# Optimization experiments

Hardware: AMD Instinct MI355X
Metric: run time of the kernel (lower is better)

The kernel has to match this reference:

```python
import jax, jax.numpy as jnp
import numpy as np

N = 50000          # masked node count
E = 800000         # edges (avg degree 16)
IN_DIM, GCN_DIM, REL_DIM, TRAIN_DIM, OUT_DIM = 3, 128, 64, 128, 2
BATCHES = 1


def setup_inputs() -> dict:
    key = jax.random.key(0)
    ks = jax.random.split(key, 16)
    s = 0.05
    return {
        "features": jax.random.normal(ks[0], (N, IN_DIM), jnp.float32),
        "edge_index": jax.random.randint(ks[1], (2, E), 0, N, dtype=jnp.int32),
        "trainOT": jax.random.normal(ks[2], (TRAIN_DIM,), jnp.float32),
        "W1": jax.random.normal(ks[3], (IN_DIM, GCN_DIM), jnp.float32) * s,
        "b1": jnp.zeros((GCN_DIM,), jnp.float32),
        "W2": jax.random.normal(ks[4], (GCN_DIM, GCN_DIM), jnp.float32) * s,
        "b2": jnp.zeros((GCN_DIM,), jnp.float32),
        "Wq": jax.random.normal(ks[5], (GCN_DIM, REL_DIM), jnp.float32) * s,
        "bq": jnp.zeros((REL_DIM,), jnp.float32),
        "Wk": jax.random.normal(ks[6], (TRAIN_DIM, REL_DIM), jnp.float32) * s,
        "bk": jnp.zeros((REL_DIM,), jnp.float32),
        "Wv": jax.random.normal(ks[7], (GCN_DIM, TRAIN_DIM), jnp.float32) * s,
        "bv": jnp.zeros((TRAIN_DIM,), jnp.float32),
        "Ws": jax.random.normal(ks[8], (TRAIN_DIM, OUT_DIM * N), jnp.float32) * s,
        "bs": jnp.zeros((OUT_DIM * N,), jnp.float32),
    }


def _gcn_conv(x, W, b, src, dst, n):
    """PyG GCNConv: h = D^-1/2 (A+I) D^-1/2 (x W) + b (self-loops already in src/dst)."""
    h = x @ W                                                  # [n, d_out]
    ones = jnp.ones(src.shape[0], dtype=x.dtype)
    deg = jax.ops.segment_sum(ones, dst, num_segments=n)      # in-degree incl. self-loop
    dinv = jnp.where(deg > 0, jax.lax.rsqrt(deg), 0.0)
    norm = dinv[src] * dinv[dst]                               # [E+n]
    msg = h[src] * norm[:, None]                               # gather (dominant traffic)
    return jax.ops.segment_sum(msg, dst, num_segments=n) + b   # scatter-add


def reference(features, edge_index, trainOT, W1, b1, W2, b2, Wq, bq, Wk, bk, Wv, bv, Ws, bs):
    n = features.shape[0]
    loop = jnp.arange(n, dtype=edge_index.dtype)
    src = jnp.concatenate([edge_index[0], loop])
    dst = jnp.concatenate([edge_index[1], loop])

    h1 = jax.nn.relu(_gcn_conv(features, W1, b1, src, dst, n))   # gcn1 + relu
    h2 = _gcn_conv(h1, W2, b2, src, dst, n)                      # gcn2

    q = h2 @ Wq + bq                                             # [n, rel]
    v = h2 @ Wv + bv                                             # [n, train]
    k = trainOT @ Wk + bk                                        # [rel]
    scale = jnp.asarray(Wq.shape[1], q.dtype) ** 0.5
    rel = jax.nn.sigmoid((q @ k) / scale)                        # [n]
    summed_idea = (rel[:, None] * v).sum(axis=0)                 # [train]
    new_trainOT = trainOT + summed_idea
    speak = new_trainOT @ Ws + bs                                # [out_dim * num_nodes]
    out = speak.reshape(BATCHES, -1, OUT_DIM)
    return out, new_trainOT
```

## Files before the change

kernel.cpp:

```cpp
#include <hip/hip_runtime.h>
#include <math.h>

#define O_RPD    (0)
#define O_RPS    (256*1024)
#define O_DINV   (512*1024)
#define O_SMALL  (768*1024)
#define O_Y      (1024*1024)
#define O_RELW   (1280*1024)
#define O_REL    (1536*1024)
#define O_GHD    (1792*1024)
#define O_GHS    (2048*1024)
#define O_GOD    (2304*1024)
#define O_GOS    (2560*1024)
#define O_BSD    (2816*1024)
#define O_BSS    (2944*1024)
#define O_PART   (3072*1024)
#define O_XS     (3712*1024)
#define O_G1     (4608*1024)
#define O_SRTD   (5632*1024)
#define O_SRTS   (9216*1024)
#define O_COLD   (12544*1024)
#define O_COLS   (16128*1024)

#define NCHUNK 256
#define ZBLOCKS 1024

static __device__ __forceinline__ int blockExclScan256(int v, volatile int* lds, int t) {
    int lane = t & 63, wid = t >> 6;
    int incl = v;
#pragma unroll
    for (int off = 1; off < 64; off <<= 1) {
        int n = __shfl_up(incl, off);
        if (lane >= off) incl += n;
    }
    if (lane == 63) lds[wid] = incl;
    __syncthreads();
    if (t == 0) {
        int s = 0;
#pragma unroll
        for (int i = 0; i < 4; ++i) { int x = lds[i]; lds[i] = s; s += x; }
    }
    __syncthreads();
    return lds[wid] + incl - v;
}

__global__ void k_hist(const int* __restrict__ eidx, int* __restrict__ ghD,
                       int* __restrict__ ghS,
                       const float* __restrict__ trainOT, const float* __restrict__ Wq,
                       const float* __restrict__ bq, const float* __restrict__ Wk,
                       const float* __restrict__ bk, const float* __restrict__ W2,
                       const float* __restrict__ b2, float* __restrict__ small,
                       int E, int CS, int NB) {
    int b = blockIdx.x, t = threadIdx.x;
    if (b == NCHUNK) {
        if (blockIdx.y) return;
        __shared__ float kv[64];
        __shared__ float wqk[128];
        __shared__ float fred[256];
        if (t < 64) {
            float acc = bk[t];
            for (int j = 0; j < 128; ++j) acc += trainOT[j] * Wk[j * 64 + t];
            kv[t] = acc;
        }
        __syncthreads();
        if (t < 128) {
            float aq = 0.f;
            for (int c2 = 0; c2 < 64; ++c2) aq += Wq[t * 64 + c2] * kv[c2];
            wqk[t] = aq;
        }
        fred[t] = (t < 64) ? bq[t] * kv[t] : 0.f;
        __syncthreads();
        for (int off = 128; off >= 1; off >>= 1) { if (t < off) fred[t] += fred[t + off]; __syncthreads(); }
        float bqs = fred[0];
        __syncthreads();
        if (t < 128) {
            float a2 = 0.f;
            for (int j = 0; j < 128; ++j) a2 += W2[t * 128 + j] * wqk[j];
            small[t] = a2;
        }
        fred[t] = (t < 128) ? b2[t] * wqk[t] : 0.f;
        __syncthreads();
        for (int off = 128; off >= 1; off >>= 1) { if (t < off) fred[t] += fred[t + off]; __syncthreads(); }
        if (t == 0) small[128] = bqs + fred[0];
        return;
    }
    __shared__ int lh[256];
    const int* arr = blockIdx.y ? eidx : (eidx + E);
    int* gh = blockIdx.y ? ghS : ghD;
    lh[t] = 0; __syncthreads();
    int s = b * CS, e = min(E, s + CS);
    for (int i = s + t; i < e; i += 256) atomicAdd(&lh[arr[i] >> 8], 1);
    __syncthreads();
    if (t < NB) gh[t * NCHUNK + b] = lh[t];
}

__global__ void k_bstart(const int* __restrict__ ghD, const int* __restrict__ ghS,
                         int* __restrict__ bsD, int* __restrict__ bsS, int NB) {
    __shared__ int lds1[4];
    __shared__ int lds2[4];
    int t = threadIdx.x;
    int vD = 0, vS = 0;
    if (t < NB) {
        const int* rD = ghD + t * NCHUNK;
        const int* rS = ghS + t * NCHUNK;
        for (int b = 0; b < NCHUNK; ++b) { vD += rD[b]; vS += rS[b]; }
    }
    int exD = blockExclScan256(vD, lds1, t);
    if (t <= NB) bsD[t] = exD;
    __syncthreads();
    int exS = blockExclScan256(vS, lds2, t);
    if (t <= NB) bsS[t] = exS;
}

__global__ void k_goff(const int* __restrict__ ghD, const int* __restrict__ ghS,
                       const int* __restrict__ bsD, const int* __restrict__ bsS,
                       int* __restrict__ goD, int* __restrict__ goS, int NB) {
    __shared__ int lds1[4];
    int nb = blockIdx.x, t = threadIdx.x;
    const int* gh = blockIdx.y ? ghS : ghD;
    const int* bs = blockIdx.y ? bsS : bsD;
    int* go = blockIdx.y ? goS : goD;
    int base = bs[nb];
    int g = gh[nb * NCHUNK + t];
    int gx = blockExclScan256(g, lds1, t);
    go[nb * NCHUNK + t] = base + gx;
}

__global__ void k_scatter(const int* __restrict__ eidx, const int* __restrict__ goD,
                          const int* __restrict__ goS, unsigned int* __restrict__ srtD,
                          unsigned int* __restrict__ srtS, int E, int CS, int NB) {
    __shared__ int lcur[256];
    int b = blockIdx.x, t = threadIdx.x;
    const int* key = blockIdx.y ? eidx : (eidx + E);
    const int* val = blockIdx.y ? (eidx + E) : eidx;
    const int* go  = blockIdx.y ? goS : goD;
    unsigned int* srt = blockIdx.y ? srtS : srtD;
    if (t < NB) lcur[t] = go[t * NCHUNK + b];
    __syncthreads();
    int s = b * CS, e = min(E, s + CS);
    for (int i = s + t; i < e; i += 256) {
        int k = key[i];
        int pos = atomicAdd(&lcur[k >> 8], 1);
        srt[pos] = ((unsigned int)(k & 255) << 16) | (unsigned int)val[i];
    }
}

__global__ void k_build(const unsigned int* __restrict__ srtD, const unsigned int* __restrict__ srtS,
                        const int* __restrict__ bsD, const int* __restrict__ bsS,
                        int* __restrict__ rpD, int* __restrict__ rpS,
                        int* __restrict__ colD, int* __restrict__ colS,
                        float* __restrict__ dinv, const float* __restrict__ x,
                        float4* __restrict__ xs4, int N, int NB) {
    __shared__ int lcnt[256];
    __shared__ int lpos[256];
    __shared__ int lds1[4];
    int nb = blockIdx.x, t = threadIdx.x;
    bool rev = blockIdx.y != 0;
    const unsigned int* srt = rev ? srtS : srtD;
    const int* bst = rev ? bsS : bsD;
    int* rp  = rev ? rpS : rpD;
    int* col = rev ? colS : colD;
    lcnt[t] = 0; __syncthreads();
    int s = bst[nb], e = bst[nb + 1];
    for (int i = s + t; i < e; i += 256) atomicAdd(&lcnt[srt[i] >> 16], 1);
    __syncthreads();
    int c = lcnt[t];
    int cx = blockExclScan256(c, lds1, t);
    int rpv = s + cx;
    int node = (nb << 8) + t;
    rp[node] = rpv;
    lpos[t] = rpv;
    if (!rev && node < N) {
        float d = rsqrtf((float)(c + 1));
        dinv[node] = d;
        float4 v;
        v.x = x[node * 3] * d; v.y = x[node * 3 + 1] * d; v.z = x[node * 3 + 2] * d; v.w = 0.f;
        xs4[node] = v;
    }
    __syncthreads();
    for (int i = s + t; i < e; i += 256) {
        unsigned int v = srt[i];
        int p = atomicAdd(&lpos[v >> 16], 1);
        col[p] = (int)(v & 0xffffu);
    }
}

__global__ void k_y(const float4* __restrict__ xs4, const int* __restrict__ rpD,
                    const int* __restrict__ colD, const float* __restrict__ dinv,
                    const float* __restrict__ W1, const float* __restrict__ b1,
                    const float* __restrict__ small, float4* __restrict__ g1,
                    float* __restrict__ y, int N) {
    int t = threadIdx.x;
    int sub = t & 15;
    int node = blockIdx.x * 16 + (t >> 4);
    if (node >= N) return;
    float di = dinv[node];
    int s = rpD[node], e = rpD[node + 1];
    float a0 = 0.f, a1 = 0.f, a2 = 0.f;
    for (int j = s + sub; j < e; j += 16) {
        float4 xv = xs4[colD[j]];
        a0 += xv.x; a1 += xv.y; a2 += xv.z;
    }
    if (sub == 0) { float4 xv = xs4[node]; a0 += xv.x; a1 += xv.y; a2 += xv.z; }
#pragma unroll
    for (int off = 1; off < 16; off <<= 1) {
        a0 += __shfl_xor(a0, off);
        a1 += __shfl_xor(a1, off);
        a2 += __shfl_xor(a2, off);
    }
    a0 *= di; a1 *= di; a2 *= di;
    float yl = 0.f;
#pragma unroll
    for (int m = 0; m < 8; ++m) {
        int c = sub * 8 + m;
        float h = fmaxf(a0 * W1[c] + a1 * W1[128 + c] + a2 * W1[256 + c] + b1[c], 0.f);
        yl += h * small[c];
    }
#pragma unroll
    for (int off = 1; off < 16; off <<= 1) yl += __shfl_xor(yl, off);
    if (sub == 0) {
        y[node] = yl * di;
        float4 gv; gv.x = a0; gv.y = a1; gv.z = a2; gv.w = di;
        g1[node] = gv;
    }
}

__global__ void k_dv(const float* __restrict__ y, const int* __restrict__ rpD,
                     const int* __restrict__ colD, const float* __restrict__ dinv,
                     const float* __restrict__ small, float* __restrict__ relw,
                     float* __restrict__ rel, int N) {
    int t = threadIdx.x;
    int sub = t & 15;
    int node = blockIdx.x * 16 + (t >> 4);
    if (node >= N) return;
    float di = dinv[node];
    int s = rpD[node], e = rpD[node + 1];
    float acc = (sub == 0) ? y[node] : 0.f;
    for (int j = s + sub; j < e; j += 16) acc += y[colD[j]];
#pragma unroll
    for (int off = 1; off < 16; off <<= 1) acc += __shfl_xor(acc, off);
    float z = (acc * di + small[128]) * 0.125f;
    float r = 1.f / (1.f + __expf(-z));
    if (sub == 0) { rel[node] = r; relw[node] = r * di; }
}

__global__ void k_z(const float4* __restrict__ g1, const int* __restrict__ rpS,
                    const int* __restrict__ colS, const float* __restrict__ relw,
                    const float* __restrict__ rel, const float* __restrict__ W1,
                    const float* __restrict__ b1, float* __restrict__ part, int N) {
    __shared__ float W1s[384];
    __shared__ float b1s[128];
    __shared__ float sS[4][132];
    int t = threadIdx.x, lane = t & 63, wid = t >> 6;
    int sub = lane & 15;
    if (t < 128) { W1s[t] = W1[t]; W1s[128 + t] = W1[128 + t]; W1s[256 + t] = W1[256 + t];
                   b1s[t] = b1[t]; }
    __syncthreads();
    float acc[8];
#pragma unroll
    for (int m = 0; m < 8; ++m) acc[m] = 0.f;
    float Racc = 0.f;
    for (int node = blockIdx.x * 16 + (t >> 4); node < N; node += ZBLOCKS * 16) {
        int s = rpS[node], e = rpS[node + 1];
        float w = (sub == 0) ? relw[node] : 0.f;
        for (int j = s + sub; j < e; j += 16) w += relw[colS[j]];
#pragma unroll
        for (int off = 1; off < 16; off <<= 1) w += __shfl_xor(w, off);
        float4 gv = g1[node];
        float zw = w * gv.w;
#pragma unroll
        for (int m = 0; m < 8; ++m) {
            int c = sub * 8 + m;
            float h = fmaxf(gv.x * W1s[c] + gv.y * W1s[128 + c] + gv.z * W1s[256 + c] + b1s[c], 0.f);
            acc[m] += zw * h;
        }
        if (sub == 0) Racc += rel[node];
    }
#pragma unroll
    for (int m = 0; m < 8; ++m) {
        acc[m] += __shfl_xor(acc[m], 16);
        acc[m] += __shfl_xor(acc[m], 32);
    }
    Racc += __shfl_xor(Racc, 16);
    Racc += __shfl_xor(Racc, 32);
    if (lane < 16) {
#pragma unroll
        for (int m = 0; m < 8; ++m) sS[wid][sub * 8 + m] = acc[m];
    }
    if (lane == 0) sS[wid][128] = Racc;
    __syncthreads();
    if (t < 129) part[blockIdx.x * 132 + t] = sS[0][t] + sS[1][t] + sS[2][t] + sS[3][t];
}

__global__ void k_reduce_part(const float* __restrict__ part, int nblocks, float* __restrict__ small) {
    int c = blockIdx.x;
    float acc = 0.f;
    for (int b = threadIdx.x; b < nblocks; b += blockDim.x) acc += part[b * 132 + c];
    __shared__ float sd[256];
    sd[threadIdx.x] = acc; __syncthreads();
    for (int off = 128; off; off >>= 1) { if (threadIdx.x < off) sd[threadIdx.x] += sd[threadIdx.x + off]; __syncthreads(); }
    if (threadIdx.x == 0) small[132 + c] = sd[0];
}

__global__ void k_tinytail(const float* __restrict__ trainOT, const float* __restrict__ W2,
                           const float* __restrict__ b2, const float* __restrict__ Wv,
                           const float* __restrict__ bv, float* __restrict__ small,
                           float* __restrict__ out_tail) {
    __shared__ float partial[1024];
    __shared__ float Ss[128];
    __shared__ float t1[128];
    int t = threadIdx.x;
    int o = t & 127, sl = t >> 7;
    if (t < 128) Ss[t] = small[132 + t];
    __syncthreads();
    float R = small[260];
    float acc = 0.f;
#pragma unroll
    for (int j = sl * 16; j < sl * 16 + 16; ++j) acc += Ss[j] * W2[j * 128 + o];
    partial[t] = acc; __syncthreads();
    if (t < 128) {
        float v = R * b2[t];
#pragma unroll
        for (int k = 0; k < 8; ++k) v += partial[t + 128 * k];
        t1[t] = v;
    }
    __syncthreads();
    float acc2 = 0.f;
#pragma unroll
    for (int j = sl * 16; j < sl * 16 + 16; ++j) acc2 += t1[j] * Wv[j * 128 + o];
    partial[t] = acc2; __syncthreads();
    if (t < 128) {
        float v = R * bv[t];
#pragma unroll
        for (int k = 0; k < 8; ++k) v += partial[t + 128 * k];
        float nt = trainOT[t] + v;
        small[264 + t] = nt;
        out_tail[t] = nt;
    }
}

__global__ void k_speak(const float* __restrict__ Ws, const float* __restrict__ bs,
                        const float* __restrict__ small, float* __restrict__ out, int out_n) {
    __shared__ float nt[128];
    __shared__ float s0[256], s1[256];
    int t = threadIdx.x;
    if (t < 128) nt[t] = small[264 + t];
    __syncthreads();
    int jj = (t & 63) * 2, sl = t >> 6;
    int j = blockIdx.x * 128 + jj;
    float a0 = 0.f, a1 = 0.f;
    if (j < out_n) {
        const float* w = Ws + (size_t)(sl * 32) * out_n + j;
        for (int k = 0; k < 32; ++k) {
            float cv = nt[sl * 32 + k];
            float2 r = *reinterpret_cast<const float2*>(w + (size_t)k * out_n);
            a0 += cv * r.x; a1 += cv * r.y;
        }
    }
    s0[t] = a0; s1[t] = a1; __syncthreads();
    if (t < 64 && j < out_n) {
        out[j]     = s0[t] + s0[t + 64] + s0[t + 128] + s0[t + 192] + bs[j];
        out[j + 1] = s1[t] + s1[t + 64] + s1[t + 128] + s1[t + 192] + bs[j + 1];
    }
}

extern "C" void kernel_launch(void* const* d_in, const int* in_sizes, int n_in,
                              void* d_out, int out_size, void* d_ws, size_t ws_size,
                              hipStream_t stream) {
    const float* features = (const float*)d_in[0];
    const int*   eidx     = (const int*)d_in[1];
    const float* trainOT  = (const float*)d_in[2];
    const float* W1 = (const float*)d_in[3];
    const float* b1 = (const float*)d_in[4];
    const float* W2 = (const float*)d_in[5];
    const float* b2 = (const float*)d_in[6];
    const float* Wq = (const float*)d_in[7];
    const float* bq = (const float*)d_in[8];
    const float* Wk = (const float*)d_in[9];
    const float* bk = (const float*)d_in[10];
    const float* Wv = (const float*)d_in[11];
    const float* bv = (const float*)d_in[12];
    const float* Ws = (const float*)d_in[13];
    const float* bs = (const float*)d_in[14];

    int N = in_sizes[0] / 3;
    int E = in_sizes[1] / 2;
    int NB = (N + 255) >> 8;
    int CS = (E + NCHUNK - 1) / NCHUNK;

    char* ws = (char*)d_ws;
    int*   rpD   = (int*)(ws + O_RPD);
    int*   rpS   = (int*)(ws + O_RPS);
    float* dinv  = (float*)(ws + O_DINV);
    float* small = (float*)(ws + O_SMALL);
    float* y     = (float*)(ws + O_Y);
    float* relw  = (float*)(ws + O_RELW);
    float* rel   = (float*)(ws + O_REL);
    int*   ghD   = (int*)(ws + O_GHD);
    int*   ghS   = (int*)(ws + O_GHS);
    int*   goD   = (int*)(ws + O_GOD);
    int*   goS   = (int*)(ws + O_GOS);
    int*   bsD   = (int*)(ws + O_BSD);
    int*   bsS   = (int*)(ws + O_BSS);
    float* part  = (float*)(ws + O_PART);
    float4* xs4  = (float4*)(ws + O_XS);
    float4* g1   = (float4*)(ws + O_G1);
    unsigned int* srtD = (unsigned int*)(ws + O_SRTD);
    unsigned int* srtS = (unsigned int*)(ws + O_SRTS);
    int*   colD  = (int*)(ws + O_COLD);
    int*   colS  = (int*)(ws + O_COLS);
    float* out   = (float*)d_out;
    int out_n = out_size - 128;

    k_hist<<<dim3(NCHUNK + 1, 2), 256, 0, stream>>>(eidx, ghD, ghS,
                                                    trainOT, Wq, bq, Wk, bk, W2, b2, small,
                                                    E, CS, NB);
    k_bstart<<<1, 256, 0, stream>>>(ghD, ghS, bsD, bsS, NB);
    k_goff<<<dim3(NB, 2), 256, 0, stream>>>(ghD, ghS, bsD, bsS, goD, goS, NB);
    k_scatter<<<dim3(NCHUNK, 2), 256, 0, stream>>>(eidx, goD, goS, srtD, srtS, E, CS, NB);
    k_build<<<dim3(NB, 2), 256, 0, stream>>>(srtD, srtS, bsD, bsS, rpD, rpS, colD, colS,
                                             dinv, features, xs4, N, NB);
    k_y<<<(N + 15) / 16, 256, 0, stream>>>(xs4, rpD, colD, dinv, W1, b1, small, g1, y, N);
    k_dv<<<(N + 15) / 16, 256, 0, stream>>>(y, rpD, colD, dinv, small, relw, rel, N);
    k_z<<<ZBLOCKS, 256, 0, stream>>>(g1, rpS, colS, relw, rel, W1, b1, part, N);
    k_reduce_part<<<129, 256, 0, stream>>>(part, ZBLOCKS, small);
    k_tinytail<<<1, 1024, 0, stream>>>(trainOT, W2, b2, Wv, bv, small, out + out_n);
    k_speak<<<(out_n + 127) / 128, 256, 0, stream>>>(Ws, bs, small, out, out_n);
}
```

Before: 104.1 us.

## Drop source-sorted CSR and fuse layer-2 pass into per-destination gather kernel

Removes the second (source-keyed) CSR build entirely and merges the k_bstart scan into k_goff. The old y/dv/z kernels, which pushed weights through the reversed graph, are replaced by one k_dvz kernel. For each destination node it recomputes relu(xW1) for every neighbour, aggregates the full 128-wide H vector, and derives rel and the weighted sum locally. This halves the sort/scatter/build work and removes two kernel launches. In exchange, each edge now costs a 3x128 recompute per node group, and the inner edge loop is serial within 16 lanes.

```diff
diff --git a/kernel.cpp b/kernel.cpp
--- a/kernel.cpp
+++ b/kernel.cpp
@@ -2,25 +2,16 @@
 #include <math.h>
 
 #define O_RPD    (0)
-#define O_RPS    (256*1024)
 #define O_DINV   (512*1024)
 #define O_SMALL  (768*1024)
-#define O_Y      (1024*1024)
-#define O_RELW   (1280*1024)
-#define O_REL    (1536*1024)
 #define O_GHD    (1792*1024)
-#define O_GHS    (2048*1024)
 #define O_GOD    (2304*1024)
-#define O_GOS    (2560*1024)
 #define O_BSD    (2816*1024)
-#define O_BSS    (2944*1024)
 #define O_PART   (3072*1024)
 #define O_XS     (3712*1024)
 #define O_G1     (4608*1024)
 #define O_SRTD   (5632*1024)
-#define O_SRTS   (9216*1024)
 #define O_COLD   (12544*1024)
-#define O_COLS   (16128*1024)
 
 #define NCHUNK 256
 #define ZBLOCKS 1024
@@ -45,7 +36,6 @@
 }
 
 __global__ void k_hist(const int* __restrict__ eidx, int* __restrict__ ghD,
-                       int* __restrict__ ghS,
                        const float* __restrict__ trainOT, const float* __restrict__ Wq,
                        const float* __restrict__ bq, const float* __restrict__ Wk,
                        const float* __restrict__ bk, const float* __restrict__ W2,
@@ -53,7 +43,6 @@
                        int E, int CS, int NB) {
     int b = blockIdx.x, t = threadIdx.x;
     if (b == NCHUNK) {
-        if (blockIdx.y) return;
         __shared__ float kv[64];
         __shared__ float wqk[128];
         __shared__ float fred[256];
@@ -85,92 +74,69 @@
         return;
     }
     __shared__ int lh[256];
-    const int* arr = blockIdx.y ? eidx : (eidx + E);
-    int* gh = blockIdx.y ? ghS : ghD;
+    const int* dst = eidx + E;
     lh[t] = 0; __syncthreads();
     int s = b * CS, e = min(E, s + CS);
-    for (int i = s + t; i < e; i += 256) atomicAdd(&lh[arr[i] >> 8], 1);
-    __syncthreads();
-    if (t < NB) gh[t * NCHUNK + b] = lh[t];
-}
-
-__global__ void k_bstart(const int* __restrict__ ghD, const int* __restrict__ ghS,
-                         int* __restrict__ bsD, int* __restrict__ bsS, int NB) {
-    __shared__ int lds1[4];
-    __shared__ int lds2[4];
-    int t = threadIdx.x;
-    int vD = 0, vS = 0;
-    if (t < NB) {
-        const int* rD = ghD + t * NCHUNK;
-        const int* rS = ghS + t * NCHUNK;
-        for (int b = 0; b < NCHUNK; ++b) { vD += rD[b]; vS += rS[b]; }
-    }
-    int exD = blockExclScan256(vD, lds1, t);
-    if (t <= NB) bsD[t] = exD;
-    __syncthreads();
-    int exS = blockExclScan256(vS, lds2, t);
-    if (t <= NB) bsS[t] = exS;
-}
-
-__global__ void k_goff(const int* __restrict__ ghD, const int* __restrict__ ghS,
-                       const int* __restrict__ bsD, const int* __restrict__ bsS,
-                       int* __restrict__ goD, int* __restrict__ goS, int NB) {
+    for (int i = s + t; i < e; i += 256) atomicAdd(&lh[dst[i] >> 8], 1);
+    __syncthreads();
+    if (t < NB) ghD[t * NCHUNK + b] = lh[t];
+}
+
+__global__ void k_goff(const int* __restrict__ ghD, int* __restrict__ goD,
+                       int* __restrict__ bsD, int E, int NB) {
+    __shared__ int lred[256];
     __shared__ int lds1[4];
     int nb = blockIdx.x, t = threadIdx.x;
-    const int* gh = blockIdx.y ? ghS : ghD;
-    const int* bs = blockIdx.y ? bsS : bsD;
-    int* go = blockIdx.y ? goS : goD;
-    int base = bs[nb];
-    int g = gh[nb * NCHUNK + t];
+    int rs = 0;
+    if (t < nb) {
+        const int4* row = reinterpret_cast<const int4*>(ghD + t * NCHUNK);
+        for (int i = 0; i < NCHUNK / 4; ++i) { int4 p = row[i]; rs += p.x + p.y + p.z + p.w; }
+    }
+    lred[t] = rs; __syncthreads();
+    for (int off = 128; off >= 1; off >>= 1) { if (t < off) lred[t] += lred[t + off]; __syncthreads(); }
+    int base = lred[0];
+    __syncthreads();
+    if (t == 0) { bsD[nb] = base; if (nb == NB - 1) bsD[NB] = E; }
+    int g = ghD[nb * NCHUNK + t];
     int gx = blockExclScan256(g, lds1, t);
-    go[nb * NCHUNK + t] = base + gx;
+    goD[nb * NCHUNK + t] = base + gx;
 }
 
 __global__ void k_scatter(const int* __restrict__ eidx, const int* __restrict__ goD,
-                          const int* __restrict__ goS, unsigned int* __restrict__ srtD,
-                          unsigned int* __restrict__ srtS, int E, int CS, int NB) {
+                          unsigned int* __restrict__ srtD, int E, int CS, int NB) {
     __shared__ int lcur[256];
     int b = blockIdx.x, t = threadIdx.x;
-    const int* key = blockIdx.y ? eidx : (eidx + E);
-    const int* val = blockIdx.y ? (eidx + E) : eidx;
-    const int* go  = blockIdx.y ? goS : goD;
-    unsigned int* srt = blockIdx.y ? srtS : srtD;
-    if (t < NB) lcur[t] = go[t * NCHUNK + b];
+    const int* dst = eidx + E;
+    const int* src = eidx;
+    if (t < NB) lcur[t] = goD[t * NCHUNK + b];
     __syncthreads();
     int s = b * CS, e = min(E, s + CS);
     for (int i = s + t; i < e; i += 256) {
-        int k = key[i];
+        int k = dst[i];
         int pos = atomicAdd(&lcur[k >> 8], 1);
-        srt[pos] = ((unsigned int)(k & 255) << 16) | (unsigned int)val[i];
-    }
-}
-
-__global__ void k_build(const unsigned int* __restrict__ srtD, const unsigned int* __restrict__ srtS,
-                        const int* __restrict__ bsD, const int* __restrict__ bsS,
-                        int* __restrict__ rpD, int* __restrict__ rpS,
-                        int* __restrict__ colD, int* __restrict__ colS,
+        srtD[pos] = ((unsigned int)(k & 255) << 16) | (unsigned int)src[i];
+    }
+}
+
+__global__ void k_build(const unsigned int* __restrict__ srtD, const int* __restrict__ bsD,
+                        int* __restrict__ rpD, int* __restrict__ colD,
                         float* __restrict__ dinv, const float* __restrict__ x,
-                        float4* __restrict__ xs4, int N, int NB) {
+                        float4* __restrict__ xs4, int N) {
     __shared__ int lcnt[256];
     __shared__ int lpos[256];
     __shared__ int lds1[4];
     int nb = blockIdx.x, t = threadIdx.x;
-    bool rev = blockIdx.y != 0;
-    const unsigned int* srt = rev ? srtS : srtD;
-    const int* bst = rev ? bsS : bsD;
-    int* rp  = rev ? rpS : rpD;
-    int* col = rev ? colS : colD;
     lcnt[t] = 0; __syncthreads();
-    int s = bst[nb], e = bst[nb + 1];
-    for (int i = s + t; i < e; i += 256) atomicAdd(&lcnt[srt[i] >> 16], 1);
+    int s = bsD[nb], e = bsD[nb + 1];
+    for (int i = s + t; i < e; i += 256) atomicAdd(&lcnt[srtD[i] >> 16], 1);
     __syncthreads();
     int c = lcnt[t];
     int cx = blockExclScan256(c, lds1, t);
     int rpv = s + cx;
     int node = (nb << 8) + t;
-    rp[node] = rpv;
+    rpD[node] = rpv;
     lpos[t] = rpv;
-    if (!rev && node < N) {
+    if (node < N) {
         float d = rsqrtf((float)(c + 1));
         dinv[node] = d;
         float4 v;
@@ -179,17 +145,15 @@
     }
     __syncthreads();
     for (int i = s + t; i < e; i += 256) {
-        unsigned int v = srt[i];
+        unsigned int v = srtD[i];
         int p = atomicAdd(&lpos[v >> 16], 1);
-        col[p] = (int)(v & 0xffffu);
-    }
-}
-
-__global__ void k_y(const float4* __restrict__ xs4, const int* __restrict__ rpD,
-                    const int* __restrict__ colD, const float* __restrict__ dinv,
-                    const float* __restrict__ W1, const float* __restrict__ b1,
-                    const float* __restrict__ small, float4* __restrict__ g1,
-                    float* __restrict__ y, int N) {
+        colD[p] = (int)(v & 0xffffu);
+    }
+}
+
+__global__ void k_g1k(const float4* __restrict__ xs4, const int* __restrict__ rpD,
+                      const int* __restrict__ colD, const float* __restrict__ dinv,
+                      float4* __restrict__ g1, int N) {
     int t = threadIdx.x;
     int sub = t & 15;
     int node = blockIdx.x * 16 + (t >> 4);
@@ -208,84 +172,77 @@
         a1 += __shfl_xor(a1, off);
         a2 += __shfl_xor(a2, off);
     }
-    a0 *= di; a1 *= di; a2 *= di;
-    float yl = 0.f;
-#pragma unroll
-    for (int m = 0; m < 8; ++m) {
-        int c = sub * 8 + m;
-        float h = fmaxf(a0 * W1[c] + a1 * W1[128 + c] + a2 * W1[256 + c] + b1[c], 0.f);
-        yl += h * small[c];
-    }
-#pragma unroll
-    for (int off = 1; off < 16; off <<= 1) yl += __shfl_xor(yl, off);
     if (sub == 0) {
-        y[node] = yl * di;
-        float4 gv; gv.x = a0; gv.y = a1; gv.z = a2; gv.w = di;
+        float4 gv; gv.x = a0 * di; gv.y = a1 * di; gv.z = a2 * di; gv.w = di;
         g1[node] = gv;
     }
 }
 
-__global__ void k_dv(const float* __restrict__ y, const int* __restrict__ rpD,
-                     const int* __restrict__ colD, const float* __restrict__ dinv,
-                     const float* __restrict__ small, float* __restrict__ relw,
-                     float* __restrict__ rel, int N) {
-    int t = threadIdx.x;
-    int sub = t & 15;
-    int node = blockIdx.x * 16 + (t >> 4);
-    if (node >= N) return;
-    float di = dinv[node];
-    int s = rpD[node], e = rpD[node + 1];
-    float acc = (sub == 0) ? y[node] : 0.f;
-    for (int j = s + sub; j < e; j += 16) acc += y[colD[j]];
-#pragma unroll
-    for (int off = 1; off < 16; off <<= 1) acc += __shfl_xor(acc, off);
-    float z = (acc * di + small[128]) * 0.125f;
-    float r = 1.f / (1.f + __expf(-z));
-    if (sub == 0) { rel[node] = r; relw[node] = r * di; }
-}
-
-__global__ void k_z(const float4* __restrict__ g1, const int* __restrict__ rpS,
-                    const int* __restrict__ colS, const float* __restrict__ relw,
-                    const float* __restrict__ rel, const float* __restrict__ W1,
-                    const float* __restrict__ b1, float* __restrict__ part, int N) {
+__global__ void k_dvz(const float4* __restrict__ g1, const int* __restrict__ rpD,
+                      const int* __restrict__ colD, const float* __restrict__ W1,
+                      const float* __restrict__ b1, const float* __restrict__ small,
+                      float* __restrict__ part, int N) {
     __shared__ float W1s[384];
     __shared__ float b1s[128];
+    __shared__ float wqs[128];
     __shared__ float sS[4][132];
     int t = threadIdx.x, lane = t & 63, wid = t >> 6;
     int sub = lane & 15;
     if (t < 128) { W1s[t] = W1[t]; W1s[128 + t] = W1[128 + t]; W1s[256 + t] = W1[256 + t];
-                   b1s[t] = b1[t]; }
-    __syncthreads();
-    float acc[8];
-#pragma unroll
-    for (int m = 0; m < 8; ++m) acc[m] = 0.f;
+                   b1s[t] = b1[t]; wqs[t] = small[t]; }
+    __syncthreads();
+    float bias = small[128];
+    float sacc[8];
+#pragma unroll
+    for (int m = 0; m < 8; ++m) sacc[m] = 0.f;
     float Racc = 0.f;
     for (int node = blockIdx.x * 16 + (t >> 4); node < N; node += ZBLOCKS * 16) {
-        int s = rpS[node], e = rpS[node + 1];
-        float w = (sub == 0) ? relw[node] : 0.f;
-        for (int j = s + sub; j < e; j += 16) w += relw[colS[j]];
-#pragma unroll
-        for (int off = 1; off < 16; off <<= 1) w += __shfl_xor(w, off);
-        float4 gv = g1[node];
-        float zw = w * gv.w;
+        float4 gs = g1[node];
+        float di = gs.w;
+        float H[8];
 #pragma unroll
         for (int m = 0; m < 8; ++m) {
             int c = sub * 8 + m;
-            float h = fmaxf(gv.x * W1s[c] + gv.y * W1s[128 + c] + gv.z * W1s[256 + c] + b1s[c], 0.f);
-            acc[m] += zw * h;
-        }
-        if (sub == 0) Racc += rel[node];
+            float h = fmaxf(gs.x * W1s[c] + gs.y * W1s[128 + c] + gs.z * W1s[256 + c] + b1s[c], 0.f);
+            H[m] = h * di;
+        }
+        int s = rpD[node], e = rpD[node + 1];
+        for (int j = s; j < e; j += 2) {
+            int u0 = colD[j];
+            float4 ga = g1[u0];
+            float4 gb;
+            if (j + 1 < e) { gb = g1[colD[j + 1]]; }
+            else { gb.x = 0.f; gb.y = 0.f; gb.z = 0.f; gb.w = 0.f; }
+#pragma unroll
+            for (int m = 0; m < 8; ++m) {
+                int c = sub * 8 + m;
+                float ha = fmaxf(ga.x * W1s[c] + ga.y * W1s[128 + c] + ga.z * W1s[256 + c] + b1s[c], 0.f);
+                float hb = fmaxf(gb.x * W1s[c] + gb.y * W1s[128 + c] + gb.z * W1s[256 + c] + b1s[c], 0.f);
+                H[m] += ha * ga.w + hb * gb.w;
+            }
+        }
+        float dv = 0.f;
+#pragma unroll
+        for (int m = 0; m < 8; ++m) dv += H[m] * wqs[sub * 8 + m];
+#pragma unroll
+        for (int off = 1; off < 16; off <<= 1) dv += __shfl_xor(dv, off);
+        float zz = (dv * di + bias) * 0.125f;
+        float rel = 1.f / (1.f + __expf(-zz));
+        float relw = rel * di;
+#pragma unroll
+        for (int m = 0; m < 8; ++m) sacc[m] += relw * H[m];
+        if (sub == 0) Racc += rel;
     }
 #pragma unroll
     for (int m = 0; m < 8; ++m) {
-        acc[m] += __shfl_xor(acc[m], 16);
-        acc[m] += __shfl_xor(acc[m], 32);
+        sacc[m] += __shfl_xor(sacc[m], 16);
+        sacc[m] += __shfl_xor(sacc[m], 32);
     }
     Racc += __shfl_xor(Racc, 16);
     Racc += __shfl_xor(Racc, 32);
     if (lane < 16) {
 #pragma unroll
-        for (int m = 0; m < 8; ++m) sS[wid][sub * 8 + m] = acc[m];
+        for (int m = 0; m < 8; ++m) sS[wid][sub * 8 + m] = sacc[m];
     }
     if (lane == 0) sS[wid][128] = Racc;
     __syncthreads();
@@ -390,39 +347,26 @@
 
     char* ws = (char*)d_ws;
     int*   rpD   = (int*)(ws + O_RPD);
-    int*   rpS   = (int*)(ws + O_RPS);
     float* dinv  = (float*)(ws + O_DINV);
     float* small = (float*)(ws + O_SMALL);
-    float* y     = (float*)(ws + O_Y);
-    float* relw  = (float*)(ws + O_RELW);
-    float* rel   = (float*)(ws + O_REL);
     int*   ghD   = (int*)(ws + O_GHD);
-    int*   ghS   = (int*)(ws + O_GHS);
     int*   goD   = (int*)(ws + O_GOD);
-    int*   goS   = (int*)(ws + O_GOS);
     int*   bsD   = (int*)(ws + O_BSD);
-    int*   bsS   = (int*)(ws + O_BSS);
     float* part  = (float*)(ws + O_PART);
     float4* xs4  = (float4*)(ws + O_XS);
     float4* g1   = (float4*)(ws + O_G1);
     unsigned int* srtD = (unsigned int*)(ws + O_SRTD);
-    unsigned int* srtS = (unsigned int*)(ws + O_SRTS);
     int*   colD  = (int*)(ws + O_COLD);
-    int*   colS  = (int*)(ws + O_COLS);
     float* out   = (float*)d_out;
     int out_n = out_size - 128;
 
-    k_hist<<<dim3(NCHUNK + 1, 2), 256, 0, stream>>>(eidx, ghD, ghS,
-                                                    trainOT, Wq, bq, Wk, bk, W2, b2, small,
-                                                    E, CS, NB);
-    k_bstart<<<1, 256, 0, stream>>>(ghD, ghS, bsD, bsS, NB);
-    k_goff<<<dim3(NB, 2), 256, 0, stream>>>(ghD, ghS, bsD, bsS, goD, goS, NB);
-    k_scatter<<<dim3(NCHUNK, 2), 256, 0, stream>>>(eidx, goD, goS, srtD, srtS, E, CS, NB);
-    k_build<<<dim3(NB, 2), 256, 0, stream>>>(srtD, srtS, bsD, bsS, rpD, rpS, colD, colS,
-                                             dinv, features, xs4, N, NB);
-    k_y<<<(N + 15) / 16, 256, 0, stream>>>(xs4, rpD, colD, dinv, W1, b1, small, g1, y, N);
-    k_dv<<<(N + 15) / 16, 256, 0, stream>>>(y, rpD, colD, dinv, small, relw, rel, N);
-    k_z<<<ZBLOCKS, 256, 0, stream>>>(g1, rpS, colS, relw, rel, W1, b1, part, N);
+    k_hist<<<NCHUNK + 1, 256, 0, stream>>>(eidx, ghD,
+                                           trainOT, Wq, bq, Wk, bk, W2, b2, small, E, CS, NB);
+    k_goff<<<NB, 256, 0, stream>>>(ghD, goD, bsD, E, NB);
+    k_scatter<<<NCHUNK, 256, 0, stream>>>(eidx, goD, srtD, E, CS, NB);
+    k_build<<<NB, 256, 0, stream>>>(srtD, bsD, rpD, colD, dinv, features, xs4, N);
+    k_g1k<<<(N + 15) / 16, 256, 0, stream>>>(xs4, rpD, colD, dinv, g1, N);
+    k_dvz<<<ZBLOCKS, 256, 0, stream>>>(g1, rpD, colD, W1, b1, small, part, N);
     k_reduce_part<<<129, 256, 0, stream>>>(part, ZBLOCKS, small);
     k_tinytail<<<1, 1024, 0, stream>>>(trainOT, W2, b2, Wv, bv, small, out + out_n);
     k_speak<<<(out_n + 127) / 128, 256, 0, stream>>>(Ws, bs, small, out, out_n);
```

Result: slower. 122.9 us (+18.0%).

## Drop reverse CSR build; aggregate by source bucket with LDS atomics

Applied to the files above, without the earlier changes.

The source-sorted CSR (rpS/colS) is no longer built. The reverse aggregation now reads the bucket-sorted source array directly and accumulates relw into a per-bucket LDS array with atomics, one block per 256-node bucket. The k_bstart kernel is folded into k_goff, which recomputes each bucket base by summing the preceding histogram rows, removing one launch and the second half of k_build. The cost is redundant row sums in k_goff that grow with bucket index, plus LDS atomic contention, and k_zS now runs only NB blocks.

```diff
diff --git a/kernel.cpp b/kernel.cpp
--- a/kernel.cpp
+++ b/kernel.cpp
@@ -2,7 +2,6 @@
 #include <math.h>
 
 #define O_RPD    (0)
-#define O_RPS    (256*1024)
 #define O_DINV   (512*1024)
 #define O_SMALL  (768*1024)
 #define O_Y      (1024*1024)
@@ -20,10 +19,8 @@
 #define O_SRTD   (5632*1024)
 #define O_SRTS   (9216*1024)
 #define O_COLD   (12544*1024)
-#define O_COLS   (16128*1024)
 
 #define NCHUNK 256
-#define ZBLOCKS 1024
 
 static __device__ __forceinline__ int blockExclScan256(int v, volatile int* lds, int t) {
     int lane = t & 63, wid = t >> 6;
@@ -94,33 +91,25 @@
     if (t < NB) gh[t * NCHUNK + b] = lh[t];
 }
 
-__global__ void k_bstart(const int* __restrict__ ghD, const int* __restrict__ ghS,
-                         int* __restrict__ bsD, int* __restrict__ bsS, int NB) {
-    __shared__ int lds1[4];
-    __shared__ int lds2[4];
-    int t = threadIdx.x;
-    int vD = 0, vS = 0;
-    if (t < NB) {
-        const int* rD = ghD + t * NCHUNK;
-        const int* rS = ghS + t * NCHUNK;
-        for (int b = 0; b < NCHUNK; ++b) { vD += rD[b]; vS += rS[b]; }
-    }
-    int exD = blockExclScan256(vD, lds1, t);
-    if (t <= NB) bsD[t] = exD;
-    __syncthreads();
-    int exS = blockExclScan256(vS, lds2, t);
-    if (t <= NB) bsS[t] = exS;
-}
-
 __global__ void k_goff(const int* __restrict__ ghD, const int* __restrict__ ghS,
-                       const int* __restrict__ bsD, const int* __restrict__ bsS,
-                       int* __restrict__ goD, int* __restrict__ goS, int NB) {
+                       int* __restrict__ goD, int* __restrict__ goS,
+                       int* __restrict__ bsD, int* __restrict__ bsS, int E, int NB) {
+    __shared__ int lred[256];
     __shared__ int lds1[4];
     int nb = blockIdx.x, t = threadIdx.x;
     const int* gh = blockIdx.y ? ghS : ghD;
-    const int* bs = blockIdx.y ? bsS : bsD;
     int* go = blockIdx.y ? goS : goD;
-    int base = bs[nb];
+    int* bs = blockIdx.y ? bsS : bsD;
+    int rs = 0;
+    if (t < nb) {
+        const int4* row = reinterpret_cast<const int4*>(gh + t * NCHUNK);
+        for (int i = 0; i < NCHUNK / 4; ++i) { int4 p = row[i]; rs += p.x + p.y + p.z + p.w; }
+    }
+    lred[t] = rs; __syncthreads();
+    for (int off = 128; off >= 1; off >>= 1) { if (t < off) lred[t] += lred[t + off]; __syncthreads(); }
+    int base = lred[0];
+    __syncthreads();
+    if (t == 0) { bs[nb] = base; if (nb == NB - 1) bs[NB] = E; }
     int g = gh[nb * NCHUNK + t];
     int gx = blockExclScan256(g, lds1, t);
     go[nb * NCHUNK + t] = base + gx;
@@ -145,32 +134,25 @@
     }
 }
 
-__global__ void k_build(const unsigned int* __restrict__ srtD, const unsigned int* __restrict__ srtS,
-                        const int* __restrict__ bsD, const int* __restrict__ bsS,
-                        int* __restrict__ rpD, int* __restrict__ rpS,
-                        int* __restrict__ colD, int* __restrict__ colS,
+__global__ void k_build(const unsigned int* __restrict__ srtD, const int* __restrict__ bsD,
+                        int* __restrict__ rpD, int* __restrict__ colD,
                         float* __restrict__ dinv, const float* __restrict__ x,
-                        float4* __restrict__ xs4, int N, int NB) {
+                        float4* __restrict__ xs4, int N) {
     __shared__ int lcnt[256];
     __shared__ int lpos[256];
     __shared__ int lds1[4];
     int nb = blockIdx.x, t = threadIdx.x;
-    bool rev = blockIdx.y != 0;
-    const unsigned int* srt = rev ? srtS : srtD;
-    const int* bst = rev ? bsS : bsD;
-    int* rp  = rev ? rpS : rpD;
-    int* col = rev ? colS : colD;
     lcnt[t] = 0; __syncthreads();
-    int s = bst[nb], e = bst[nb + 1];
-    for (int i = s + t; i < e; i += 256) atomicAdd(&lcnt[srt[i] >> 16], 1);
+    int s = bsD[nb], e = bsD[nb + 1];
+    for (int i = s + t; i < e; i += 256) atomicAdd(&lcnt[srtD[i] >> 16], 1);
     __syncthreads();
     int c = lcnt[t];
     int cx = blockExclScan256(c, lds1, t);
     int rpv = s + cx;
     int node = (nb << 8) + t;
-    rp[node] = rpv;
+    rpD[node] = rpv;
     lpos[t] = rpv;
-    if (!rev && node < N) {
+    if (node < N) {
         float d = rsqrtf((float)(c + 1));
         dinv[node] = d;
         float4 v;
@@ -179,9 +161,9 @@
     }
     __syncthreads();
     for (int i = s + t; i < e; i += 256) {
-        unsigned int v = srt[i];
+        unsigned int v = srtD[i];
         int p = atomicAdd(&lpos[v >> 16], 1);
-        col[p] = (int)(v & 0xffffu);
+        colD[p] = (int)(v & 0xffffu);
     }
 }
 
@@ -244,52 +226,61 @@
     if (sub == 0) { rel[node] = r; relw[node] = r * di; }
 }
 
-__global__ void k_z(const float4* __restrict__ g1, const int* __restrict__ rpS,
-                    const int* __restrict__ colS, const float* __restrict__ relw,
-                    const float* __restrict__ rel, const float* __restrict__ W1,
-                    const float* __restrict__ b1, float* __restrict__ part, int N) {
+__global__ void k_zS(const unsigned int* __restrict__ srtS, const int* __restrict__ bsS,
+                     const float* __restrict__ relw, const float* __restrict__ rel,
+                     const float4* __restrict__ g1, const float* __restrict__ W1,
+                     const float* __restrict__ b1, float* __restrict__ part, int N) {
+    __shared__ float zl[256];
     __shared__ float W1s[384];
     __shared__ float b1s[128];
     __shared__ float sS[4][132];
-    int t = threadIdx.x, lane = t & 63, wid = t >> 6;
-    int sub = lane & 15;
+    int nb = blockIdx.x, t = threadIdx.x, lane = t & 63, wid = t >> 6;
+    int sub = lane & 15, gid = wid * 4 + (lane >> 4);
+    int node0 = (nb << 8) + t;
+    zl[t] = (node0 < N) ? relw[node0] : 0.f;
     if (t < 128) { W1s[t] = W1[t]; W1s[128 + t] = W1[128 + t]; W1s[256 + t] = W1[256 + t];
                    b1s[t] = b1[t]; }
     __syncthreads();
-    float acc[8];
-#pragma unroll
-    for (int m = 0; m < 8; ++m) acc[m] = 0.f;
+    int s = bsS[nb], e = bsS[nb + 1];
+    for (int i = s + t; i < e; i += 256) {
+        unsigned int v = srtS[i];
+        atomicAdd(&zl[v >> 16], relw[v & 0xffffu]);
+    }
+    __syncthreads();
+    float sacc[8];
+#pragma unroll
+    for (int m = 0; m < 8; ++m) sacc[m] = 0.f;
     float Racc = 0.f;
-    for (int node = blockIdx.x * 16 + (t >> 4); node < N; node += ZBLOCKS * 16) {
-        int s = rpS[node], e = rpS[node + 1];
-        float w = (sub == 0) ? relw[node] : 0.f;
-        for (int j = s + sub; j < e; j += 16) w += relw[colS[j]];
-#pragma unroll
-        for (int off = 1; off < 16; off <<= 1) w += __shfl_xor(w, off);
-        float4 gv = g1[node];
-        float zw = w * gv.w;
-#pragma unroll
-        for (int m = 0; m < 8; ++m) {
-            int c = sub * 8 + m;
-            float h = fmaxf(gv.x * W1s[c] + gv.y * W1s[128 + c] + gv.z * W1s[256 + c] + b1s[c], 0.f);
-            acc[m] += zw * h;
+#pragma unroll 4
+    for (int r = 0; r < 16; ++r) {
+        int nl = gid * 16 + r;
+        int node = (nb << 8) + nl;
+        if (node < N) {
+            float4 gv = g1[node];
+            float zw = zl[nl] * gv.w;
+#pragma unroll
+            for (int m = 0; m < 8; ++m) {
+                int c = sub * 8 + m;
+                float h = fmaxf(gv.x * W1s[c] + gv.y * W1s[128 + c] + gv.z * W1s[256 + c] + b1s[c], 0.f);
+                sacc[m] += zw * h;
+            }
+            if (sub == 0) Racc += rel[node];
         }
-        if (sub == 0) Racc += rel[node];
     }
 #pragma unroll
     for (int m = 0; m < 8; ++m) {
-        acc[m] += __shfl_xor(acc[m], 16);
-        acc[m] += __shfl_xor(acc[m], 32);
+        sacc[m] += __shfl_xor(sacc[m], 16);
+        sacc[m] += __shfl_xor(sacc[m], 32);
     }
     Racc += __shfl_xor(Racc, 16);
     Racc += __shfl_xor(Racc, 32);
     if (lane < 16) {
 #pragma unroll
-        for (int m = 0; m < 8; ++m) sS[wid][sub * 8 + m] = acc[m];
+        for (int m = 0; m < 8; ++m) sS[wid][sub * 8 + m] = sacc[m];
     }
     if (lane == 0) sS[wid][128] = Racc;
     __syncthreads();
-    if (t < 129) part[blockIdx.x * 132 + t] = sS[0][t] + sS[1][t] + sS[2][t] + sS[3][t];
+    if (t < 129) part[nb * 132 + t] = sS[0][t] + sS[1][t] + sS[2][t] + sS[3][t];
 }
 
 __global__ void k_reduce_part(const float* __restrict__ part, int nblocks, float* __restrict__ small) {
@@ -390,7 +381,6 @@
 
     char* ws = (char*)d_ws;
     int*   rpD   = (int*)(ws + O_RPD);
-    int*   rpS   = (int*)(ws + O_RPS);
     float* dinv  = (float*)(ws + O_DINV);
     float* small = (float*)(ws + O_SMALL);
     float* y     = (float*)(ws + O_Y);
@@ -408,22 +398,19 @@
     unsigned int* srtD = (unsigned int*)(ws + O_SRTD);
     unsigned int* srtS = (unsigned int*)(ws + O_SRTS);
     int*   colD  = (int*)(ws + O_COLD);
-    int*   colS  = (int*)(ws + O_COLS);
     float* out   = (float*)d_out;
     int out_n = out_size - 128;
 
     k_hist<<<dim3(NCHUNK + 1, 2), 256, 0, stream>>>(eidx, ghD, ghS,
                                                     trainOT, Wq, bq, Wk, bk, W2, b2, small,
                                                     E, CS, NB);
-    k_bstart<<<1, 256, 0, stream>>>(ghD, ghS, bsD, bsS, NB);
-    k_goff<<<dim3(NB, 2), 256, 0, stream>>>(ghD, ghS, bsD, bsS, goD, goS, NB);
+    k_goff<<<dim3(NB, 2), 256, 0, stream>>>(ghD, ghS, goD, goS, bsD, bsS, E, NB);
     k_scatter<<<dim3(NCHUNK, 2), 256, 0, stream>>>(eidx, goD, goS, srtD, srtS, E, CS, NB);
-    k_build<<<dim3(NB, 2), 256, 0, stream>>>(srtD, srtS, bsD, bsS, rpD, rpS, colD, colS,
-                                             dinv, features, xs4, N, NB);
+    k_build<<<NB, 256, 0, stream>>>(srtD, bsD, rpD, colD, dinv, features, xs4, N);
     k_y<<<(N + 15) / 16, 256, 0, stream>>>(xs4, rpD, colD, dinv, W1, b1, small, g1, y, N);
     k_dv<<<(N + 15) / 16, 256, 0, stream>>>(y, rpD, colD, dinv, small, relw, rel, N);
-    k_z<<<ZBLOCKS, 256, 0, stream>>>(g1, rpS, colS, relw, rel, W1, b1, part, N);
-    k_reduce_part<<<129, 256, 0, stream>>>(part, ZBLOCKS, small);
+    k_zS<<<NB, 256, 0, stream>>>(srtS, bsS, relw, rel, g1, W1, b1, part, N);
+    k_reduce_part<<<129, 256, 0, stream>>>(part, NB, small);
     k_tinytail<<<1, 1024, 0, stream>>>(trainOT, W2, b2, Wv, bv, small, out + out_n);
     k_speak<<<(out_n + 127) / 128, 256, 0, stream>>>(Ws, bs, small, out, out_n);
 }
```

Measured after the change: 98.84 us, median of 2. 1.05x faster.
